# Optimization experiments

Measured on AMD Instinct MI355X. Metric: run time of the kernel, lower is better.

The kernel has to match this reference:

```python
import jax, jax.numpy as jnp
import numpy as np
from jax import lax

N_NODES = 10000
IN_DIM = 144
OUT_DIM = 700
THETA_DIM = 256
TOP_K = 5
BN_EPS = 1e-5
LRELU_SLOPE = 0.01


def setup_inputs() -> dict:
    key = jax.random.key(0)
    ks = jax.random.split(key, 5)
    return {
        "H": jax.random.normal(ks[0], (N_NODES, IN_DIM), dtype=jnp.float32),
        "bn_gamma": jnp.ones((IN_DIM,), jnp.float32),
        "bn_beta": jnp.zeros((IN_DIM,), jnp.float32),
        "W_theta": jax.random.normal(ks[1], (IN_DIM, THETA_DIM), jnp.float32) * (1.0 / np.sqrt(IN_DIM)),
        "b_theta": jax.random.normal(ks[2], (THETA_DIM,), jnp.float32) * 0.01,
        "W_out": jax.random.normal(ks[3], (IN_DIM, OUT_DIM), jnp.float32) * (1.0 / np.sqrt(IN_DIM)),
        "b_out": jax.random.normal(ks[4], (OUT_DIM,), jnp.float32) * 0.01,
    }


def _forward(H, bn_gamma, bn_beta, W_theta, b_theta, W_out, b_out):
    # BatchNorm1d over nodes (training-mode batch statistics, biased variance)
    mean = H.mean(axis=0)
    var = ((H - mean) ** 2).mean(axis=0)
    Hn = (H - mean) * lax.rsqrt(var + BN_EPS) * bn_gamma + bn_beta

    # theta projection -> SAM (spectral angle) adjacency; torch code detaches here
    Hx = Hn @ W_theta + b_theta                                  # [n, 256]
    Xn = Hx / jnp.maximum(jnp.linalg.norm(Hx, axis=1, keepdims=True), 1e-12)
    cos = jnp.clip(Xn @ Xn.T, -1.0, 1.0)                         # [n, n]
    sam = jnp.nan_to_num(jnp.arccos(cos))
    A = jnp.clip(jax.nn.sigmoid(jnp.exp(-0.2 * sam)), 0.1, None)
    A = lax.stop_gradient(A)  # SAM() goes through .detach() in torch

    # per-row top-k=5 mask (argsort(-A) first k columns)
    _, idx = lax.top_k(A, TOP_K)                                  # [n, k]
    n = A.shape[0]
    mask = jnp.zeros_like(A).at[jnp.arange(n)[:, None], idx].set(1.0)
    A = A * mask

    # symmetric normalization D^-0.5 A D^-0.5 (diagonal mm as row/col scaling)
    d = A.sum(axis=1) ** -0.5                                     # [n]
    A_hat = A * d[:, None] * d[None, :]

    out = A_hat @ (Hn @ W_out + b_out)                            # [n, out_dim]
    out = jnp.where(out >= 0, out, LRELU_SLOPE * out)             # LeakyReLU
    return out, A


def reference(H, bn_gamma, bn_beta, W_theta, b_theta, W_out, b_out):
    return _forward(H, bn_gamma, bn_beta, W_theta, b_theta, W_out, b_out)
```

## Files before the change

kernel.cpp:

```cpp
#include <hip/hip_runtime.h>
#include <hip/hip_bf16.h>
#include <math.h>

#define N_NODES 10000
#define NPAD2   10240
#define IN_DIM  144
#define TD      256
#define OD      700
#define TOPK    5
#define GK      160
#define GLD     168
#define LDT     72

typedef __attribute__((ext_vector_type(8))) short short8v;
typedef __attribute__((ext_vector_type(4))) float f32x4;

__device__ inline unsigned short f32_to_bf16_rne(float f){
    unsigned int u = __float_as_uint(f);
    unsigned int r = u + 0x7fffu + ((u >> 16) & 1u);
    return (unsigned short)(r >> 16);
}

__global__ void bn_partial(const float* __restrict__ H, double* __restrict__ part){
    int c = threadIdx.x;
    int b = blockIdx.x;
    if (c >= IN_DIM) return;
    int r0 = b * 80;
    double s = 0.0, q = 0.0;
    #pragma unroll 4
    for (int r = r0; r < r0 + 80; ++r){
        double v = (double)H[r*IN_DIM + c];
        s += v; q += v*v;
    }
    part[b*288 + c]       = s;
    part[b*288 + 144 + c] = q;
}

__global__ void bn_finish(const double* __restrict__ part, double* __restrict__ stats){
    int c = threadIdx.x;
    if (c >= 288) return;
    double s = 0.0;
    for (int b = 0; b < 125; ++b) s += part[b*288 + c];
    stats[c] = s;
}

__global__ __launch_bounds__(256) void theta_kernel(
    const float* __restrict__ H, const float* __restrict__ gam, const float* __restrict__ bet,
    const float* __restrict__ Wt, const float* __restrict__ bt, const double* __restrict__ stats,
    float* __restrict__ Xn32, unsigned short* __restrict__ Xh, unsigned short* __restrict__ Hn16)
{
    __shared__ double hn[4][IN_DIM];
    __shared__ double red[4][4];
    __shared__ double invs[4];
    int tid = threadIdx.x;
    int r0 = blockIdx.x * 4;

    if (tid < GK){
        int c = tid;
        bool real = (c < IN_DIM);
        double mean = 0.0, scale = 0.0, bb = 0.0;
        if (real){
            mean  = stats[c] * (1.0/10000.0);
            double var = stats[144+c] * (1.0/10000.0) - mean*mean;
            scale = (1.0/sqrt(var + 1e-5)) * (double)gam[c];
            bb    = (double)bet[c];
        }
        for (int r = 0; r < 4; ++r){
            int row = r0 + r;
            float vf = 0.0f;
            if (real && row < N_NODES)
                vf = (float)(((double)H[row*IN_DIM + c] - mean)*scale + bb);
            if (row < 10048) Hn16[(size_t)row*GK + c] = f32_to_bf16_rne(vf);
            if (real) hn[r][c] = (double)vf;
        }
    }
    __syncthreads();

    int j = tid;
    double a0,a1,a2,a3;
    a0=a1=a2=a3=(double)bt[j];
    for (int k = 0; k < IN_DIM; ++k){
        double w = (double)Wt[k*TD + j];
        a0 += hn[0][k]*w; a1 += hn[1][k]*w; a2 += hn[2][k]*w; a3 += hn[3][k]*w;
    }
    float hx0=(float)a0, hx1=(float)a1, hx2=(float)a2, hx3=(float)a3;
    double n0=(double)hx0*(double)hx0, n1=(double)hx1*(double)hx1,
           n2=(double)hx2*(double)hx2, n3=(double)hx3*(double)hx3;
    #pragma unroll
    for (int off=32; off>0; off>>=1){
        n0 += __shfl_down(n0, off);
        n1 += __shfl_down(n1, off);
        n2 += __shfl_down(n2, off);
        n3 += __shfl_down(n3, off);
    }
    int lane = tid & 63, wave = tid >> 6;
    if (lane == 0){ red[0][wave]=n0; red[1][wave]=n1; red[2][wave]=n2; red[3][wave]=n3; }
    __syncthreads();
    if (tid < 4){
        double s = red[tid][0]+red[tid][1]+red[tid][2]+red[tid][3];
        invs[tid] = 1.0 / fmax(sqrt(s), 1e-12);
    }
    __syncthreads();

    float hx[4] = {hx0,hx1,hx2,hx3};
    #pragma unroll
    for (int r = 0; r < 4; ++r){
        int row = r0 + r;
        float xn = 0.0f;
        if (row < N_NODES) xn = (float)((double)hx[r]*invs[r]);
        Xn32[(size_t)row*TD + j] = xn;
        Xh  [(size_t)row*TD + j] = f32_to_bf16_rne(xn);
    }
}

__global__ __launch_bounds__(256) void wconv(const float* __restrict__ Wo,
                                             unsigned short* __restrict__ WoT16)
{
    int j = blockIdx.x;
    int k = threadIdx.x;
    if (k >= GK) return;
    float v = (j < OD && k < IN_DIM) ? Wo[k*OD + j] : 0.0f;
    WoT16[(size_t)j*GK + k] = f32_to_bf16_rne(v);
}

__global__ __launch_bounds__(256,2) void gproj(const unsigned short* __restrict__ Hn16,
    const unsigned short* __restrict__ WoT16, const float* __restrict__ bo,
    float* __restrict__ G)
{
    __shared__ short Al[64*GLD];
    __shared__ short Wl[2][64*GLD];
    int tid = threadIdx.x;
    int w = tid >> 6, lane = tid & 63;
    int l15 = lane & 15, l4 = lane >> 4;
    int i0 = blockIdx.x * 64;

    int sr = tid >> 2, sc = tid & 3;
    #pragma unroll
    for (int p = 0; p < 5; ++p){
        int cb = sc + (p<<2);
        *(short8v*)(&Al[sr*GLD + cb*8]) =
            *(const short8v*)(&Hn16[(size_t)(i0+sr)*GK + cb*8]);
    }
    #pragma unroll
    for (int p = 0; p < 5; ++p){
        int cb = sc + (p<<2);
        *(short8v*)(&Wl[0][sr*GLD + cb*8]) =
            *(const short8v*)(&WoT16[(size_t)sr*GK + cb*8]);
    }
    __syncthreads();

    for (int jt = 0; jt < 11; ++jt){
        int cur = jt & 1;
        bool pf = (jt < 10);
        short8v g[5];
        if (pf){
            #pragma unroll
            for (int p = 0; p < 5; ++p){
                int cb = sc + (p<<2);
                g[p] = *(const short8v*)(&WoT16[(size_t)((jt+1)*64 + sr)*GK + cb*8]);
            }
        }
        f32x4 acc[4];
        #pragma unroll
        for (int n=0;n<4;++n) acc[n] = (f32x4){0.f,0.f,0.f,0.f};
        #pragma unroll
        for (int ks = 0; ks < 5; ++ks){
            short8v af = *(const short8v*)(&Al[(w*16 + l15)*GLD + ks*32 + l4*8]);
            #pragma unroll
            for (int n=0;n<4;++n){
                short8v bf = *(const short8v*)(&Wl[cur][(n*16 + l15)*GLD + ks*32 + l4*8]);
                acc[n] = __builtin_amdgcn_mfma_f32_16x16x32_bf16(af, bf, acc[n], 0, 0, 0);
            }
        }
        #pragma unroll
        for (int n=0;n<4;++n){
            int jcol = jt*64 + n*16 + l15;
            if (jcol < OD){
                float b = bo[jcol];
                #pragma unroll
                for (int q=0;q<4;++q){
                    int irow = i0 + w*16 + l4*4 + q;
                    if (irow < N_NODES)
                        G[(size_t)irow*OD + jcol] = acc[n][q] + b;
                }
            }
        }
        if (pf){
            #pragma unroll
            for (int p = 0; p < 5; ++p){
                int cb = sc + (p<<2);
                *(short8v*)(&Wl[cur^1][sr*GLD + cb*8]) = g[p];
            }
        }
        __syncthreads();
    }
}

__global__ __launch_bounds__(256,3) void cos_blk(const unsigned short* __restrict__ Xh,
                                                 unsigned int* __restrict__ pkey)
{
    __shared__ unsigned int smem[10240];
    short* Al = (short*)smem;
    short* Bl = ((short*)smem) + 128*LDT;

    int t = blockIdx.x;
    int bi = 0, rem = t;
    while (rem >= 80 - bi){ rem -= 80 - bi; ++bi; }
    int bj = bi + rem;
    int i0 = bi * 128;
    int j0 = bj * 128;

    int tid = threadIdx.x;
    int w = tid >> 6, lane = tid & 63;
    int l15 = lane & 15, l4 = lane >> 4;

    f32x4 acc[2][8];
    #pragma unroll
    for (int jf=0;jf<2;++jf){
        #pragma unroll
        for (int f=0;f<8;++f) acc[jf][f] = (f32x4){0.f,0.f,0.f,0.f};
    }

    int str = tid >> 3;
    int scb = tid & 7;

    for (int kc = 0; kc < TD; kc += 64){
        __syncthreads();
        #pragma unroll
        for (int p=0;p<4;++p){
            int r = p*32 + str;
            *(short8v*)(&Al[r*LDT + scb*8]) =
                *(const short8v*)(&Xh[(size_t)(i0+r)*TD + kc + scb*8]);
            *(short8v*)(&Bl[r*LDT + scb*8]) =
                *(const short8v*)(&Xh[(size_t)(j0+r)*TD + kc + scb*8]);
        }
        __syncthreads();
        #pragma unroll
        for (int ks=0; ks<2; ++ks){
            short8v af0 = *(const short8v*)(&Bl[(w*32 +  0 + l15)*LDT + ks*32 + l4*8]);
            short8v af1 = *(const short8v*)(&Bl[(w*32 + 16 + l15)*LDT + ks*32 + l4*8]);
            #pragma unroll
            for (int f=0; f<8; ++f){
                short8v bf = *(const short8v*)(&Al[(f*16 + l15)*LDT + ks*32 + l4*8]);
                acc[0][f] = __builtin_amdgcn_mfma_f32_16x16x32_bf16(af0, bf, acc[0][f], 0,0,0);
                acc[1][f] = __builtin_amdgcn_mfma_f32_16x16x32_bf16(af1, bf, acc[1][f], 0,0,0);
            }
        }
    }
    __syncthreads();

    unsigned int* lists = smem;

    #pragma unroll
    for (int f=0; f<8; ++f){
        unsigned int t5[5] = {0u,0u,0u,0u,0u};
        #pragma unroll
        for (int jf=0; jf<2; ++jf){
            #pragma unroll
            for (int q=0; q<4; ++q){
                float v = acc[jf][f][q];
                int jl = w*32 + jf*16 + l4*4 + q;
                unsigned int u = __float_as_uint(v);
                unsigned int key = ((int)u < 0) ? ~u : (u | 0x80000000u);
                unsigned int pk = (key & 0xFFFFFF80u) | (unsigned int)(127 - jl);
                if (pk > t5[4]){
                    t5[4] = pk;
                    #pragma unroll
                    for (int s=4;s>0;--s){
                        if (t5[s] > t5[s-1]){ unsigned int tp=t5[s]; t5[s]=t5[s-1]; t5[s-1]=tp; }
                    }
                }
            }
        }
        int row  = f*16 + l15;
        int base = row*80 + (w*4 + l4)*5;
        #pragma unroll
        for (int s=0;s<5;++s) lists[base+s] = t5[s];
    }
    __syncthreads();

    if (tid < 128){
        unsigned int b5[5] = {0u,0u,0u,0u,0u};
        int rb = tid*80;
        for (int c=0;c<80;++c){
            unsigned int pk = lists[rb + c];
            if (pk > b5[4]){
                b5[4] = pk;
                #pragma unroll
                for (int s=4;s>0;--s){
                    if (b5[s] > b5[s-1]){ unsigned int tp=b5[s]; b5[s]=b5[s-1]; b5[s-1]=tp; }
                }
            }
        }
        size_t gb = (size_t)(i0 + tid)*400 + (size_t)bj*5;
        #pragma unroll
        for (int s=0;s<5;++s) pkey[gb + s] = b5[s];
    }

    if (bi == bj) return;

    __syncthreads();

    #pragma unroll
    for (int jf=0; jf<2; ++jf){
        #pragma unroll
        for (int q=0; q<4; ++q){
            unsigned int t5[5] = {0u,0u,0u,0u,0u};
            #pragma unroll
            for (int f=0; f<8; ++f){
                float v = acc[jf][f][q];
                int il = f*16 + l15;
                unsigned int u = __float_as_uint(v);
                unsigned int key = ((int)u < 0) ? ~u : (u | 0x80000000u);
                unsigned int pk = (key & 0xFFFFFF80u) | (unsigned int)(127 - il);
                if (pk > t5[4]){
                    t5[4] = pk;
                    #pragma unroll
                    for (int s=4;s>0;--s){
                        if (t5[s] > t5[s-1]){ unsigned int tp=t5[s]; t5[s]=t5[s-1]; t5[s-1]=tp; }
                    }
                }
            }
            int jl   = w*32 + jf*16 + l4*4 + q;
            int base = jl*80 + l15*5;
            #pragma unroll
            for (int s=0;s<5;++s) lists[base+s] = t5[s];
        }
    }
    __syncthreads();

    if (tid < 128){
        unsigned int b5[5] = {0u,0u,0u,0u,0u};
        int rb = tid*80;
        for (int c=0;c<80;++c){
            unsigned int pk = lists[rb + c];
            if (pk > b5[4]){
                b5[4] = pk;
                #pragma unroll
                for (int s=4;s>0;--s){
                    if (b5[s] > b5[s-1]){ unsigned int tp=b5[s]; b5[s]=b5[s-1]; b5[s-1]=tp; }
                }
            }
        }
        size_t gb = (size_t)(j0 + tid)*400 + (size_t)bi*5;
        #pragma unroll
        for (int s=0;s<5;++s) pkey[gb + s] = b5[s];
    }
}

__global__ __launch_bounds__(64) void merge_topk(const unsigned int* __restrict__ pkey,
                                                 int* __restrict__ pidx)
{
    __shared__ unsigned int sk[400];
    int row = blockIdx.x, l = threadIdx.x;
    const unsigned int* pr = &pkey[(size_t)row*400];
    for (int t = l; t < 400; t += 64) sk[t] = pr[t];
    __syncthreads();
    for (int s=0; s<16; ++s){
        unsigned int bk = 0u; int bj = 0x7fffffff; int bslot = -1;
        for (int t = l; t < 400; t += 64){
            unsigned int k = sk[t];
            int gj = (t/5)*128 + 127 - (int)(k & 127u);
            if (k > bk || (k == bk && gj < bj)){ bk = k; bj = gj; bslot = t; }
        }
        unsigned int v = bk; int ix = bj;
        #pragma unroll
        for (int off=32; off>0; off>>=1){
            unsigned int ov = (unsigned int)__shfl_xor((int)v, off);
            int oj = __shfl_xor(ix, off);
            if (ov > v || (ov == v && oj < ix)){ v = ov; ix = oj; }
        }
        if (l == 0) pidx[(size_t)row*16 + s] = ix;
        if (bk == v && bj == ix && bslot >= 0) sk[bslot] = 0u;
        __syncthreads();
    }
}

__global__ __launch_bounds__(64) void refine(const float* __restrict__ Xn32,
    const int* __restrict__ pidx, float* __restrict__ topA, int* __restrict__ topI,
    float* __restrict__ dinv)
{
    __shared__ float xi[4][TD];
    int l = threadIdx.x;
    int grp = l >> 4, slot = l & 15;
    int row0 = blockIdx.x * 4;
    for (int t = l; t < 4*TD; t += 64)
        xi[t>>8][t&255] = Xn32[(size_t)(row0 + (t>>8))*TD + (t&255)];
    __syncthreads();

    int row = row0 + grp;
    int j  = pidx[(size_t)row*16 + slot];
    int jc = j < N_NODES ? j : 0;
    const float* xj = &Xn32[(size_t)jc*TD];
    const float* xr = xi[grp];
    double s = 0.0;
    for (int k = 0; k < TD; k += 4){
        float4 b = *(const float4*)(&xj[k]);
        s += (double)xr[k+0]*(double)b.x;
        s += (double)xr[k+1]*(double)b.y;
        s += (double)xr[k+2]*(double)b.z;
        s += (double)xr[k+3]*(double)b.w;
    }
    float cos32 = (float)s;
    cos32 = fminf(fmaxf(cos32, -1.0f), 1.0f);
    float sam = acosf(cos32);
    float e   = expf(-0.2f*sam);
    float key = 1.0f/(1.0f + expf(-e));
    if (j >= N_NODES) key = -1.0f;

    double dsum = 0.0;
    for (int t = 0; t < TOPK; ++t){
        float v = key; int ix = j;
        #pragma unroll
        for (int off=8; off>0; off>>=1){
            float ov = __shfl_xor(v, off);
            int oix  = __shfl_xor(ix, off);
            if (ov > v || (ov == v && oix < ix)){ v = ov; ix = oix; }
        }
        dsum += (double)v;
        if (slot == 0){ topA[row*TOPK + t] = v; topI[row*TOPK + t] = ix; }
        if (j == ix) key = -1.0f;
    }
    if (slot == 0) dinv[row] = (float)(1.0/sqrt(dsum));
}

__global__ __launch_bounds__(256) void outk(const float* __restrict__ G,
    const float* __restrict__ topA, const int* __restrict__ topI,
    const float* __restrict__ dinv, float* __restrict__ out)
{
    __shared__ float w[TOPK];
    __shared__ int   jj[TOPK];
    int row = blockIdx.x, tid = threadIdx.x;
    if (tid < TOPK){
        int j = topI[row*TOPK + tid];
        jj[tid] = j;
        w[tid]  = topA[row*TOPK + tid] * dinv[row] * dinv[j];
    }
    __syncthreads();
    for (int col = tid; col < OD; col += 256){
        float acc = 0.f;
        #pragma unroll
        for (int m=0;m<TOPK;++m) acc = fmaf(w[m], G[(size_t)jj[m]*OD + col], acc);
        out[(size_t)row*OD + col] = acc >= 0.f ? acc : 0.01f*acc;
    }
}

__global__ __launch_bounds__(256) void zero_scatter(const float* __restrict__ topA,
    const int* __restrict__ topI, float* __restrict__ Aout)
{
    int row = blockIdx.x;
    float4* rowp = (float4*)(Aout + (size_t)row*N_NODES);
    const float4 z = {0.f,0.f,0.f,0.f};
    int tid = threadIdx.x;
    #pragma unroll
    for (int p = 0; p < 10; ++p){
        int c = p*256 + tid;
        if (c < 2500) rowp[c] = z;
    }
    __syncthreads();
    if (tid < TOPK)
        Aout[(size_t)row*N_NODES + topI[row*TOPK + tid]] = topA[row*TOPK + tid];
}

extern "C" void kernel_launch(void* const* d_in, const int* in_sizes, int n_in,
                              void* d_out, int out_size, void* d_ws, size_t ws_size,
                              hipStream_t stream)
{
    const float* H   = (const float*)d_in[0];
    const float* gam = (const float*)d_in[1];
    const float* bet = (const float*)d_in[2];
    const float* Wt  = (const float*)d_in[3];
    const float* bt  = (const float*)d_in[4];
    const float* Wo  = (const float*)d_in[5];
    const float* bo  = (const float*)d_in[6];

    float* out  = (float*)d_out;
    float* Aout = out + (size_t)N_NODES*OD;

    float*          Xn32  = Aout;
    unsigned short* Xh    = (unsigned short*)(Aout + 2621440);
    unsigned short* Hn16  = (unsigned short*)(Aout + 3932160);
    unsigned short* WoT16 = (unsigned short*)(Aout + 4736000);
    float*          G     = Aout + 4792320;
    unsigned int*   pkey  = (unsigned int*)(Aout + 11792320);
    int*            pidx  = (int*)(Aout + 15888320);
    double*         bn_part = (double*)(Aout + 16048320);

    double* bn_stats = (double*)d_ws;
    float*  topA  = (float*)(bn_stats + 288);
    int*    topI  = (int*)(topA + 50000);
    float*  dinvp = (float*)(topI + 50000);

    bn_partial  <<<125, 192, 0, stream>>>(H, bn_part);
    bn_finish   <<<1, 320, 0, stream>>>(bn_part, bn_stats);
    theta_kernel<<<NPAD2/4, 256, 0, stream>>>(H, gam, bet, Wt, bt, bn_stats, Xn32, Xh, Hn16);
    wconv       <<<704, 256, 0, stream>>>(Wo, WoT16);
    gproj       <<<157, 256, 0, stream>>>(Hn16, WoT16, bo, G);
    cos_blk     <<<3240, 256, 0, stream>>>(Xh, pkey);
    merge_topk  <<<N_NODES, 64, 0, stream>>>(pkey, pidx);
    refine      <<<2500, 64, 0, stream>>>(Xn32, pidx, topA, topI, dinvp);
    outk        <<<N_NODES, 256, 0, stream>>>(G, topA, topI, dinvp, out);
    zero_scatter<<<N_NODES, 256, 0, stream>>>(topA, topI, Aout);
}
```

Before: 419.7 us.

## Fuse weight conversion, top-k merge/refine, and output/scatter kernels

Folds the W_out transpose-to-bf16 conversion into theta_kernel, merges merge_topk and refine into a single select_topk kernel that keeps the 16 candidates in shared memory, and fuses outk with the A zero-fill and scatter into finalize. G is moved into the workspace when it is large enough, so finalize can overwrite the A output region without clobbering G. The goal is fewer kernel launches and less intermediate global traffic. If the workspace is too small, the code falls back to the old separate kernels.

```diff
diff --git a/kernel.cpp b/kernel.cpp
--- a/kernel.cpp
+++ b/kernel.cpp
@@ -47,6 +47,7 @@
 __global__ __launch_bounds__(256) void theta_kernel(
     const float* __restrict__ H, const float* __restrict__ gam, const float* __restrict__ bet,
     const float* __restrict__ Wt, const float* __restrict__ bt, const double* __restrict__ stats,
+    const float* __restrict__ Wo, unsigned short* __restrict__ WoT16,
     float* __restrict__ Xn32, unsigned short* __restrict__ Xh, unsigned short* __restrict__ Hn16)
 {
     __shared__ double hn[4][IN_DIM];
@@ -54,6 +55,12 @@
     __shared__ double invs[4];
     int tid = threadIdx.x;
     int r0 = blockIdx.x * 4;
+
+    if (blockIdx.x < 704 && tid < GK){
+        int jj = blockIdx.x;
+        float v = (jj < OD && tid < IN_DIM) ? Wo[tid*OD + jj] : 0.0f;
+        WoT16[(size_t)jj*GK + tid] = f32_to_bf16_rne(v);
+    }
 
     if (tid < GK){
         int c = tid;
@@ -111,16 +118,6 @@
         Xn32[(size_t)row*TD + j] = xn;
         Xh  [(size_t)row*TD + j] = f32_to_bf16_rne(xn);
     }
-}
-
-__global__ __launch_bounds__(256) void wconv(const float* __restrict__ Wo,
-                                             unsigned short* __restrict__ WoT16)
-{
-    int j = blockIdx.x;
-    int k = threadIdx.x;
-    if (k >= GK) return;
-    float v = (j < OD && k < IN_DIM) ? Wo[k*OD + j] : 0.0f;
-    WoT16[(size_t)j*GK + k] = f32_to_bf16_rne(v);
 }
 
 __global__ __launch_bounds__(256,2) void gproj(const unsigned short* __restrict__ Hn16,
@@ -348,14 +345,19 @@
     }
 }
 
-__global__ __launch_bounds__(64) void merge_topk(const unsigned int* __restrict__ pkey,
-                                                 int* __restrict__ pidx)
+__global__ __launch_bounds__(64) void select_topk(const unsigned int* __restrict__ pkey,
+    const float* __restrict__ Xn32, float* __restrict__ topA, int* __restrict__ topI,
+    float* __restrict__ dinv)
 {
     __shared__ unsigned int sk[400];
+    __shared__ float xi[TD];
+    __shared__ int cand[16];
     int row = blockIdx.x, l = threadIdx.x;
     const unsigned int* pr = &pkey[(size_t)row*400];
     for (int t = l; t < 400; t += 64) sk[t] = pr[t];
-    __syncthreads();
+    for (int k = l; k < TD; k += 64) xi[k] = Xn32[(size_t)row*TD + k];
+    __syncthreads();
+
     for (int s=0; s<16; ++s){
         unsigned int bk = 0u; int bj = 0x7fffffff; int bslot = -1;
         for (int t = l; t < 400; t += 64){
@@ -370,37 +372,28 @@
             int oj = __shfl_xor(ix, off);
             if (ov > v || (ov == v && oj < ix)){ v = ov; ix = oj; }
         }
-        if (l == 0) pidx[(size_t)row*16 + s] = ix;
+        if (l == 0) cand[s] = ix;
         if (bk == v && bj == ix && bslot >= 0) sk[bslot] = 0u;
         __syncthreads();
     }
-}
-
-__global__ __launch_bounds__(64) void refine(const float* __restrict__ Xn32,
-    const int* __restrict__ pidx, float* __restrict__ topA, int* __restrict__ topI,
-    float* __restrict__ dinv)
-{
-    __shared__ float xi[4][TD];
-    int l = threadIdx.x;
-    int grp = l >> 4, slot = l & 15;
-    int row0 = blockIdx.x * 4;
-    for (int t = l; t < 4*TD; t += 64)
-        xi[t>>8][t&255] = Xn32[(size_t)(row0 + (t>>8))*TD + (t&255)];
-    __syncthreads();
-
-    int row = row0 + grp;
-    int j  = pidx[(size_t)row*16 + slot];
+
+    int c = l >> 2, p = l & 3;
+    int j  = cand[c];
     int jc = j < N_NODES ? j : 0;
-    const float* xj = &Xn32[(size_t)jc*TD];
-    const float* xr = xi[grp];
+    const float* xj = &Xn32[(size_t)jc*TD + p*64];
+    const float* xr = &xi[p*64];
     double s = 0.0;
-    for (int k = 0; k < TD; k += 4){
+    for (int k = 0; k < 64; k += 4){
         float4 b = *(const float4*)(&xj[k]);
-        s += (double)xr[k+0]*(double)b.x;
-        s += (double)xr[k+1]*(double)b.y;
-        s += (double)xr[k+2]*(double)b.z;
-        s += (double)xr[k+3]*(double)b.w;
-    }
+        float4 a = *(const float4*)(&xr[k]);
+        s += (double)a.x*(double)b.x;
+        s += (double)a.y*(double)b.y;
+        s += (double)a.z*(double)b.z;
+        s += (double)a.w*(double)b.w;
+    }
+    s += __shfl_xor(s, 1);
+    s += __shfl_xor(s, 2);
+
     float cos32 = (float)s;
     cos32 = fminf(fmaxf(cos32, -1.0f), 1.0f);
     float sam = acosf(cos32);
@@ -412,16 +405,53 @@
     for (int t = 0; t < TOPK; ++t){
         float v = key; int ix = j;
         #pragma unroll
-        for (int off=8; off>0; off>>=1){
+        for (int off=32; off>0; off>>=1){
             float ov = __shfl_xor(v, off);
             int oix  = __shfl_xor(ix, off);
             if (ov > v || (ov == v && oix < ix)){ v = ov; ix = oix; }
         }
         dsum += (double)v;
-        if (slot == 0){ topA[row*TOPK + t] = v; topI[row*TOPK + t] = ix; }
+        if (l == 0){ topA[row*TOPK + t] = v; topI[row*TOPK + t] = ix; }
         if (j == ix) key = -1.0f;
     }
-    if (slot == 0) dinv[row] = (float)(1.0/sqrt(dsum));
+    if (l == 0) dinv[row] = (float)(1.0/sqrt(dsum));
+}
+
+__global__ __launch_bounds__(256) void finalize(const float* __restrict__ G,
+    const float* __restrict__ topA, const int* __restrict__ topI,
+    const float* __restrict__ dinv, float* __restrict__ out, float* __restrict__ Aout)
+{
+    __shared__ float w[TOPK];
+    __shared__ int   jj[TOPK];
+    __shared__ float av[TOPK];
+    int row = blockIdx.x, tid = threadIdx.x;
+    if (tid < TOPK){
+        int j = topI[row*TOPK + tid];
+        float a = topA[row*TOPK + tid];
+        jj[tid] = j;
+        av[tid] = a;
+        w[tid]  = a * dinv[row] * dinv[j];
+    }
+    __syncthreads();
+
+    float4* rowp = (float4*)(Aout + (size_t)row*N_NODES);
+    const float4 z = {0.f,0.f,0.f,0.f};
+    #pragma unroll
+    for (int p = 0; p < 10; ++p){
+        int c = p*256 + tid;
+        if (c < 2500) rowp[c] = z;
+    }
+
+    for (int col = tid; col < OD; col += 256){
+        float acc = 0.f;
+        #pragma unroll
+        for (int m=0;m<TOPK;++m) acc = fmaf(w[m], G[(size_t)jj[m]*OD + col], acc);
+        out[(size_t)row*OD + col] = acc >= 0.f ? acc : 0.01f*acc;
+    }
+
+    __syncthreads();
+    if (tid < TOPK)
+        Aout[(size_t)row*N_NODES + jj[tid]] = av[tid];
 }
 
 __global__ __launch_bounds__(256) void outk(const float* __restrict__ G,
@@ -481,24 +511,31 @@
     unsigned short* Xh    = (unsigned short*)(Aout + 2621440);
     unsigned short* Hn16  = (unsigned short*)(Aout + 3932160);
     unsigned short* WoT16 = (unsigned short*)(Aout + 4736000);
-    float*          G     = Aout + 4792320;
+    float*          G_A   = Aout + 4792320;
     unsigned int*   pkey  = (unsigned int*)(Aout + 11792320);
-    int*            pidx  = (int*)(Aout + 15888320);
-    double*         bn_part = (double*)(Aout + 16048320);
+    double*         bn_part = (double*)(Aout + 15888320);
 
     double* bn_stats = (double*)d_ws;
-    float*  topA  = (float*)(bn_stats + 288);
-    int*    topI  = (int*)(topA + 50000);
-    float*  dinvp = (float*)(topI + 50000);
+    float*  topA  = (float*)d_ws + 576;
+    int*    topI  = (int*)((float*)d_ws + 50576);
+    float*  dinvp = (float*)d_ws + 100576;
+    float*  G_ws  = (float*)d_ws + 110576;
+
+    const size_t wsNeed = (size_t)(110576 + 7000000) * 4;
+    const bool gInWs = (ws_size >= wsNeed);
+    float* G = gInWs ? G_ws : G_A;
 
     bn_partial  <<<125, 192, 0, stream>>>(H, bn_part);
     bn_finish   <<<1, 320, 0, stream>>>(bn_part, bn_stats);
-    theta_kernel<<<NPAD2/4, 256, 0, stream>>>(H, gam, bet, Wt, bt, bn_stats, Xn32, Xh, Hn16);
-    wconv       <<<704, 256, 0, stream>>>(Wo, WoT16);
+    theta_kernel<<<NPAD2/4, 256, 0, stream>>>(H, gam, bet, Wt, bt, bn_stats, Wo, WoT16,
+                                              Xn32, Xh, Hn16);
     gproj       <<<157, 256, 0, stream>>>(Hn16, WoT16, bo, G);
     cos_blk     <<<3240, 256, 0, stream>>>(Xh, pkey);
-    merge_topk  <<<N_NODES, 64, 0, stream>>>(pkey, pidx);
-    refine      <<<2500, 64, 0, stream>>>(Xn32, pidx, topA, topI, dinvp);
-    outk        <<<N_NODES, 256, 0, stream>>>(G, topA, topI, dinvp, out);
-    zero_scatter<<<N_NODES, 256, 0, stream>>>(topA, topI, Aout);
-}
+    select_topk <<<N_NODES, 64, 0, stream>>>(pkey, Xn32, topA, topI, dinvp);
+    if (gInWs){
+        finalize    <<<N_NODES, 256, 0, stream>>>(G, topA, topI, dinvp, out, Aout);
+    } else {
+        outk        <<<N_NODES, 256, 0, stream>>>(G, topA, topI, dinvp, out);
+        zero_scatter<<<N_NODES, 256, 0, stream>>>(topA, topI, Aout);
+    }
+}
```

Measured after the change: 399.2 us. 1.05x faster.
